# Performance work log

Hardware: AMD Instinct MI355X
Metric: run time of the kernel (lower is better)

## Reference

```python
import jax, jax.numpy as jnp
import numpy as np

N_NODES = 100000
N_EDGES = 6400000
N_FEAT = 128
HIDDEN = 16
N_CLASSES = 10
N_GRAPHS = 1024


def setup_inputs() -> dict:
    key = jax.random.key(0)
    ks = jax.random.split(key, 16)
    x = jax.random.normal(ks[0], (N_NODES, N_FEAT), dtype=jnp.float32)
    src = jax.random.randint(ks[1], (N_EDGES,), 0, N_NODES, dtype=jnp.int64)
    dst = jax.random.randint(ks[2], (N_EDGES,), 0, N_NODES, dtype=jnp.int64)
    edge_index = jnp.stack([src, dst], axis=0)
    batch = jnp.sort(jax.random.randint(ks[3], (N_NODES,), 0, N_GRAPHS, dtype=jnp.int64))
    s = 0.1
    emb = jax.random.normal(ks[4], (N_FEAT, HIDDEN), dtype=jnp.float32) * s
    W1l = jax.random.normal(ks[5], (HIDDEN, HIDDEN), dtype=jnp.float32) * s
    b1 = jnp.zeros((HIDDEN,), dtype=jnp.float32)
    W1r = jax.random.normal(ks[6], (HIDDEN, HIDDEN), dtype=jnp.float32) * s
    W2l = jax.random.normal(ks[7], (HIDDEN, HIDDEN), dtype=jnp.float32) * s
    b2 = jnp.zeros((HIDDEN,), dtype=jnp.float32)
    W2r = jax.random.normal(ks[8], (HIDDEN, HIDDEN), dtype=jnp.float32) * s
    W3l = jax.random.normal(ks[9], (N_CLASSES, HIDDEN), dtype=jnp.float32) * s
    b3 = jnp.zeros((N_CLASSES,), dtype=jnp.float32)
    W3r = jax.random.normal(ks[10], (N_CLASSES, HIDDEN), dtype=jnp.float32) * s
    return {"x": x, "edge_index": edge_index, "batch": batch, "emb": emb,
            "W1l": W1l, "b1": b1, "W1r": W1r,
            "W2l": W2l, "b2": b2, "W2r": W2r,
            "W3l": W3l, "b3": b3, "W3r": W3r}


def _sage_conv(h, src, dst, Wl, bl, Wr, n_nodes):
    # PyG SAGEConv (aggr='mean'): out = lin_l(mean_j x_j) + lin_r(x_i), then L2-normalize
    msgs = h[src]                                             # [E, F]
    agg = jax.ops.segment_sum(msgs, dst, num_segments=n_nodes)
    deg = jax.ops.segment_sum(jnp.ones((src.shape[0],), h.dtype), dst, num_segments=n_nodes)
    agg = agg / jnp.maximum(deg, 1.0)[:, None]
    out = agg @ Wl.T + bl + h @ Wr.T
    norm = jnp.linalg.norm(out, axis=-1, keepdims=True)
    return out / jnp.maximum(norm, 1e-12)


def reference(x, edge_index, batch, emb, W1l, b1, W1r, W2l, b2, W2r, W3l, b3, W3r):
    src, dst = edge_index[0], edge_index[1]
    n = x.shape[0]
    # embedding of argmax over one-hot-ish features
    h = emb[jnp.argmax(x, axis=1)]                            # [N, H]
    h = jax.nn.relu(_sage_conv(h, src, dst, W1l, b1, W1r, n))  # dropout is identity in eval
    h = jax.nn.relu(_sage_conv(h, src, dst, W2l, b2, W2r, n))
    h = _sage_conv(h, src, dst, W3l, b3, W3r, n)              # [N, C]
    # global mean pool over graphs
    pooled = jax.ops.segment_sum(h, batch, num_segments=N_GRAPHS)
    cnt = jax.ops.segment_sum(jnp.ones((n,), h.dtype), batch, num_segments=N_GRAPHS)
    pooled = pooled / jnp.maximum(cnt, 1.0)[:, None]
    return jax.nn.softmax(pooled, axis=1)
```

## Files before the change

kernel.cpp:

```cpp
#include <hip/hip_runtime.h>
#include <hip/hip_bf16.h>

#define N_FEAT 128
#define HID 16
#define NCLS 10
#define NGRAPH 1024
#define SHIFT 7
#define NBMAX 1024
#define CAP 9216
#define CH 8192
#define EPB (CH / 256)
#define EPB2 (CH / 512)
#define GC_NODES 64
#define GCAP2 5120

__device__ __forceinline__ float u2f(unsigned int u) {
    union { unsigned int u; float f; } c; c.u = u; return c.f;
}
__device__ __forceinline__ float bf2f(__hip_bfloat16 b) {
    return __bfloat162float(b);
}
__device__ __forceinline__ unsigned short f2us(float f) {
    union { __hip_bfloat16 b; unsigned short u; } c;
    c.b = __float2bfloat16(f);
    return c.u;
}
__device__ __forceinline__ float ldw(const void* __restrict__ p, int i, int isbf) {
    return isbf ? bf2f(((const __hip_bfloat16*)p)[i]) : ((const float*)p)[i];
}
__device__ __forceinline__ void unp8(uint4 v, float* f) {
    f[0] = u2f(v.x << 16); f[1] = u2f(v.x & 0xffff0000u);
    f[2] = u2f(v.y << 16); f[3] = u2f(v.y & 0xffff0000u);
    f[4] = u2f(v.z << 16); f[5] = u2f(v.z & 0xffff0000u);
    f[6] = u2f(v.w << 16); f[7] = u2f(v.w & 0xffff0000u);
}
__device__ __forceinline__ void acc8(uint4 v, float* a8) {
    a8[0] += u2f(v.x << 16); a8[1] += u2f(v.x & 0xffff0000u);
    a8[2] += u2f(v.y << 16); a8[3] += u2f(v.y & 0xffff0000u);
    a8[4] += u2f(v.z << 16); a8[5] += u2f(v.z & 0xffff0000u);
    a8[6] += u2f(v.w << 16); a8[7] += u2f(v.w & 0xffff0000u);
}

__global__ void k_detect(const int* __restrict__ ei,
                         const unsigned int* __restrict__ xw,
                         int* __restrict__ flags) {
    if (blockIdx.x == 0 && threadIdx.x == 0) {
        int nz = 0;
        for (int i = 1; i < 256; i += 2) nz |= ei[i];
        flags[0] = (nz == 0) ? 1 : 0;
        int cnt = 0;
        for (int i = 0; i < 64; i++) {
            unsigned int ef = xw[i] & 0x7F80u;
            if (ef >= 0x3C00u && ef <= 0x4080u) cnt++;
        }
        flags[1] = (cnt >= 32) ? 1 : 0;
    }
}

__global__ void k_argmax_embed(const void* __restrict__ x,
                               const void* __restrict__ emb,
                               const int* __restrict__ flags,
                               unsigned short* __restrict__ h, int n) {
    int wave = (int)((blockIdx.x * (unsigned)blockDim.x + threadIdx.x) >> 6);
    int lane = threadIdx.x & 63;
    if (wave >= n) return;
    int isbf = flags[1];
    float v0, v1;
    if (isbf) {
        const unsigned int* row =
            (const unsigned int*)((const __hip_bfloat16*)x + (size_t)wave * N_FEAT);
        unsigned int u = row[lane];
        v0 = u2f(u << 16);
        v1 = u2f(u & 0xffff0000u);
    } else {
        const float2* row = (const float2*)((const float*)x + (size_t)wave * N_FEAT);
        float2 u = row[lane];
        v0 = u.x; v1 = u.y;
    }
    float bv; int bi;
    if (v1 > v0) { bv = v1; bi = 2 * lane + 1; }
    else         { bv = v0; bi = 2 * lane; }
    #pragma unroll
    for (int off = 1; off < 64; off <<= 1) {
        float ov = __shfl_xor(bv, off);
        int   oi = __shfl_xor(bi, off);
        if (ov > bv || (ov == bv && oi < bi)) { bv = ov; bi = oi; }
    }
    if (lane < HID) {
        unsigned short us;
        if (isbf) us = ((const unsigned short*)emb)[bi * HID + lane];
        else      us = f2us(((const float*)emb)[bi * HID + lane]);
        h[(size_t)wave * HID + lane] = us;
    }
}

__global__ void k_binhist(const int* __restrict__ ei, const int* __restrict__ flags,
                          int* __restrict__ rbBuf, int e, int nbins) {
    __shared__ int lh[NBMAX];
    int t = threadIdx.x;
    for (int b = t; b < nbins; b += 256) lh[b] = 0;
    __syncthreads();
    int base = blockIdx.x * CH;
    int sh = flags[0];
    for (int j = 0; j < EPB; j++) {
        int i = base + j * 256 + t;
        if (i < e) {
            int d = ei[((size_t)(e + i)) << sh];
            atomicAdd(&lh[d >> SHIFT], 1);
        }
    }
    __syncthreads();
    int* row = rbBuf + (size_t)blockIdx.x * nbins;
    for (int b = t; b < nbins; b += 256) row[b] = lh[b];
}

__global__ void k_colscan(int* __restrict__ rbBuf, int* __restrict__ binCnt,
                          int nblk, int nbins) {
    __shared__ int ls[1024];
    int b = blockIdx.x, t = threadIdx.x;
    int v = (t < nblk) ? rbBuf[(size_t)t * nbins + b] : 0;
    ls[t] = v;
    __syncthreads();
    #pragma unroll
    for (int off = 1; off < 1024; off <<= 1) {
        int w = (t >= off) ? ls[t - off] : 0;
        __syncthreads();
        ls[t] += w;
        __syncthreads();
    }
    if (t < nblk) rbBuf[(size_t)t * nbins + b] = ls[t] - v;
    if (t == 1023) binCnt[b] = ls[t];
}

__global__ void k_scanbins(const int* __restrict__ binCnt,
                           int* __restrict__ binStart, int nbins, int e) {
    __shared__ int ls[1024];
    int t = threadIdx.x;
    int v = (t < nbins) ? binCnt[t] : 0;
    ls[t] = v;
    __syncthreads();
    #pragma unroll
    for (int off = 1; off < 1024; off <<= 1) {
        int w = (t >= off) ? ls[t - off] : 0;
        __syncthreads();
        ls[t] += w;
        __syncthreads();
    }
    if (t < nbins) binStart[t] = ls[t] - v;
    if (t == 0) binStart[nbins] = e;
}

__global__ __launch_bounds__(512) void k_binplace(
        const int* __restrict__ ei, const int* __restrict__ flags,
        const int* __restrict__ binStart, const int* __restrict__ rbBuf,
        int* __restrict__ col, int e, int nbins) {
    __shared__ int cnt[NBMAX];
    __shared__ int ldsOff[NBMAX];
    __shared__ int ldsBase[NBMAX];
    __shared__ int ps[512];
    __shared__ int stage[CH];
    __shared__ unsigned short binOf[CH];
    int t = threadIdx.x;
    for (int b = t; b < nbins; b += 512) cnt[b] = 0;
    __syncthreads();
    int base = blockIdx.x * CH;
    int sh = flags[0];
    int myV[EPB2]; short myB[EPB2];
    for (int j = 0; j < EPB2; j++) {
        int i = base + j * 512 + t;
        if (i < e) {
            int s = ei[((size_t)i) << sh];
            int d = ei[((size_t)(e + i)) << sh];
            myV[j] = (s << SHIFT) | (d & ((1 << SHIFT) - 1));
            int b2 = d >> SHIFT;
            myB[j] = (short)b2;
            atomicAdd(&cnt[b2], 1);
        } else myB[j] = -1;
    }
    __syncthreads();
    int c[2]; int lsum = 0;
    int bb = t * 2;
    #pragma unroll
    for (int k = 0; k < 2; k++) {
        int b2 = bb + k;
        c[k] = (b2 < nbins) ? cnt[b2] : 0;
        lsum += c[k];
    }
    ps[t] = lsum;
    __syncthreads();
    #pragma unroll
    for (int off = 1; off < 512; off <<= 1) {
        int w = (t >= off) ? ps[t - off] : 0;
        __syncthreads();
        ps[t] += w;
        __syncthreads();
    }
    int run = ps[t] - lsum;
    #pragma unroll
    for (int k = 0; k < 2; k++) {
        int b2 = bb + k;
        if (b2 < nbins) ldsOff[b2] = run;
        run += c[k];
    }
    __syncthreads();
    const int* rb = rbBuf + (size_t)blockIdx.x * nbins;
    for (int b2 = t; b2 < nbins; b2 += 512) {
        ldsBase[b2] = binStart[b2] + rb[b2] - ldsOff[b2];
        cnt[b2] = 0;
    }
    __syncthreads();
    for (int j = 0; j < EPB2; j++) {
        if (myB[j] >= 0) {
            int b2 = myB[j];
            int r = atomicAdd(&cnt[b2], 1);
            int p = ldsOff[b2] + r;
            stage[p] = myV[j];
            binOf[p] = (unsigned short)b2;
        }
    }
    __syncthreads();
    int total = e - base;
    if (total > CH) total = CH;
    for (int i = t; i < total; i += 512) {
        int b2 = binOf[i];
        col[ldsBase[b2] + i] = stage[i];
    }
}

__global__ __launch_bounds__(512) void k_place(
        int* __restrict__ col, const int* __restrict__ binStart,
        int* __restrict__ rowStart, int n, int e) {
    __shared__ int stage[CAP];
    __shared__ int cntN[1 << SHIFT];
    __shared__ int sc[1 << SHIFT];
    __shared__ int rs[1 << SHIFT];
    int b = blockIdx.x;
    int t = threadIdx.x;
    int nb = b << SHIFT;
    int s0 = binStart[b];
    int s1 = binStart[b + 1];
    int cnt = s1 - s0;
    if (t < (1 << SHIFT)) cntN[t] = 0;
    bool st = (cnt <= CAP);
    __syncthreads();
    for (int i = t; i < cnt; i += 512) {
        int v = col[s0 + i];
        if (st) stage[i] = v;
        atomicAdd(&cntN[v & ((1 << SHIFT) - 1)], 1);
    }
    __syncthreads();
    if (t < (1 << SHIFT)) sc[t] = cntN[t];
    __syncthreads();
    #pragma unroll
    for (int off = 1; off < (1 << SHIFT); off <<= 1) {
        int w = 0;
        if (t < (1 << SHIFT) && t >= off) w = sc[t - off];
        __syncthreads();
        if (t < (1 << SHIFT)) sc[t] += w;
        __syncthreads();
    }
    if (t < (1 << SHIFT)) {
        int start = s0 + sc[t] - cntN[t];
        rs[t] = start;
        int node = nb + t;
        if (node < n) rowStart[node] = start;
        cntN[t] = 0;
    }
    __syncthreads();
    for (int i = t; i < cnt; i += 512) {
        int v = st ? stage[i] : col[s0 + i];
        int dl = v & ((1 << SHIFT) - 1);
        int r = atomicAdd(&cntN[dl], 1);
        col[rs[dl] + r] = v >> SHIFT;
    }
}

__global__ __launch_bounds__(256) void k_gc(
        const int* __restrict__ col, const int* __restrict__ rowStart,
        const unsigned short* __restrict__ hin,
        const void* __restrict__ Wl, const void* __restrict__ bia,
        const void* __restrict__ Wr, const int* __restrict__ flags,
        unsigned short* __restrict__ hout, int n, int e) {
    __shared__ int ecol[GCAP2];
    __shared__ float wl[HID][HID], wr[HID][HID], bb[HID];
    int t = threadIdx.x;
    int b = blockIdx.x;
    int isbf = flags[1];
    if (t < HID * HID) {
        wl[t >> 4][t & 15] = ldw(Wl, t, isbf);
        wr[t >> 4][t & 15] = ldw(Wr, t, isbf);
    }
    if (t < HID) bb[t] = ldw(bia, t, isbf);
    int nb = b * GC_NODES;
    int s0 = rowStart[nb];
    int s1 = (nb + GC_NODES < n) ? rowStart[nb + GC_NODES] : e;
    int nl = t >> 2;
    int q  = t & 3;
    int node = nb + nl;
    bool act = (node < n);
    int lo = 0, hi = 0;
    if (act) {
        lo = rowStart[node];
        hi = (node + 1 < n) ? rowStart[node + 1] : e;
    }
    const uint4* h4 = (const uint4*)hin;
    uint4 sv0, sv1;
    if (act && q == 0) {
        sv0 = h4[(size_t)node * 2];
        sv1 = h4[(size_t)node * 2 + 1];
    }
    int cnt = s1 - s0;
    bool st = (cnt <= GCAP2);
    if (st)
        for (int i = t; i < cnt; i += 256)
            ecol[i] = __builtin_nontemporal_load(col + s0 + i);
    __syncthreads();
    if (!act) return;

    float a16[16];
    #pragma unroll
    for (int k = 0; k < 16; k++) a16[k] = 0.0f;
    if (st) {
        int i = lo - s0 + q;
        int end = hi - s0;
        for (; i + 12 < end; i += 16) {
            int e0 = ecol[i], e1 = ecol[i + 4], e2 = ecol[i + 8], e3 = ecol[i + 12];
            uint4 va0 = h4[(size_t)e0 * 2],     vb0 = h4[(size_t)e0 * 2 + 1];
            uint4 va1 = h4[(size_t)e1 * 2],     vb1 = h4[(size_t)e1 * 2 + 1];
            uint4 va2 = h4[(size_t)e2 * 2],     vb2 = h4[(size_t)e2 * 2 + 1];
            uint4 va3 = h4[(size_t)e3 * 2],     vb3 = h4[(size_t)e3 * 2 + 1];
            acc8(va0, a16); acc8(vb0, a16 + 8);
            acc8(va1, a16); acc8(vb1, a16 + 8);
            acc8(va2, a16); acc8(vb2, a16 + 8);
            acc8(va3, a16); acc8(vb3, a16 + 8);
        }
        for (; i < end; i += 4) {
            int s = ecol[i];
            uint4 va = h4[(size_t)s * 2], vb = h4[(size_t)s * 2 + 1];
            acc8(va, a16); acc8(vb, a16 + 8);
        }
    } else {
        int i = lo + q;
        for (; i + 12 < hi; i += 16) {
            int e0 = col[i], e1 = col[i + 4], e2 = col[i + 8], e3 = col[i + 12];
            uint4 va0 = h4[(size_t)e0 * 2],     vb0 = h4[(size_t)e0 * 2 + 1];
            uint4 va1 = h4[(size_t)e1 * 2],     vb1 = h4[(size_t)e1 * 2 + 1];
            uint4 va2 = h4[(size_t)e2 * 2],     vb2 = h4[(size_t)e2 * 2 + 1];
            uint4 va3 = h4[(size_t)e3 * 2],     vb3 = h4[(size_t)e3 * 2 + 1];
            acc8(va0, a16); acc8(vb0, a16 + 8);
            acc8(va1, a16); acc8(vb1, a16 + 8);
            acc8(va2, a16); acc8(vb2, a16 + 8);
            acc8(va3, a16); acc8(vb3, a16 + 8);
        }
        for (; i < hi; i += 4) {
            int s = col[i];
            uint4 va = h4[(size_t)s * 2], vb = h4[(size_t)s * 2 + 1];
            acc8(va, a16); acc8(vb, a16 + 8);
        }
    }
    #pragma unroll
    for (int k = 0; k < 16; k++) a16[k] += __shfl_xor(a16[k], 1);
    #pragma unroll
    for (int k = 0; k < 16; k++) a16[k] += __shfl_xor(a16[k], 2);
    if (q == 0) {
        float invd = 1.0f / fmaxf((float)(hi - lo), 1.0f);
        #pragma unroll
        for (int k = 0; k < 16; k++) a16[k] *= invd;
        float hb[HID];
        unp8(sv0, hb);
        unp8(sv1, hb + 8);
        float o[HID]; float sq = 0.0f;
        #pragma unroll
        for (int f = 0; f < HID; f++) {
            float acc = bb[f];
            #pragma unroll
            for (int k = 0; k < HID; k++)
                acc += a16[k] * wl[f][k] + hb[k] * wr[f][k];
            o[f] = acc;
            sq += acc * acc;
        }
        float inn = 1.0f / fmaxf(sqrtf(sq), 1e-12f);
        uint4 w0, w1;
        unsigned int* wp0 = (unsigned int*)&w0;
        unsigned int* wp1 = (unsigned int*)&w1;
        #pragma unroll
        for (int v = 0; v < 4; v++) {
            unsigned int l0 = f2us(fmaxf(o[2 * v] * inn, 0.0f));
            unsigned int h0 = f2us(fmaxf(o[2 * v + 1] * inn, 0.0f));
            wp0[v] = l0 | (h0 << 16);
            unsigned int l1 = f2us(fmaxf(o[8 + 2 * v] * inn, 0.0f));
            unsigned int h1 = f2us(fmaxf(o[8 + 2 * v + 1] * inn, 0.0f));
            wp1[v] = l1 | (h1 << 16);
        }
        ((uint4*)hout)[(size_t)node * 2]     = w0;
        ((uint4*)hout)[(size_t)node * 2 + 1] = w1;
    }
}

__global__ __launch_bounds__(256) void k_gc3(
        const int* __restrict__ col, const int* __restrict__ rowStart,
        const unsigned short* __restrict__ hin,
        const void* __restrict__ Wl, const void* __restrict__ bia,
        const void* __restrict__ Wr, const int* __restrict__ flags,
        float* __restrict__ h3, int n, int e) {
    __shared__ int ecol[GCAP2];
    __shared__ float wl[NCLS][HID], wr[NCLS][HID], bb[NCLS];
    int t = threadIdx.x;
    int b = blockIdx.x;
    int isbf = flags[1];
    if (t < NCLS * HID) {
        wl[t >> 4][t & 15] = ldw(Wl, t, isbf);
        wr[t >> 4][t & 15] = ldw(Wr, t, isbf);
    }
    if (t < NCLS) bb[t] = ldw(bia, t, isbf);
    int nb = b * GC_NODES;
    int s0 = rowStart[nb];
    int s1 = (nb + GC_NODES < n) ? rowStart[nb + GC_NODES] : e;
    int nl = t >> 2;
    int q  = t & 3;
    int node = nb + nl;
    bool act = (node < n);
    int lo = 0, hi = 0;
    if (act) {
        lo = rowStart[node];
        hi = (node + 1 < n) ? rowStart[node + 1] : e;
    }
    const uint4* h4 = (const uint4*)hin;
    uint4 sv0, sv1;
    if (act && q == 0) {
        sv0 = h4[(size_t)node * 2];
        sv1 = h4[(size_t)node * 2 + 1];
    }
    int cnt = s1 - s0;
    bool st = (cnt <= GCAP2);
    if (st)
        for (int i = t; i < cnt; i += 256)
            ecol[i] = __builtin_nontemporal_load(col + s0 + i);
    __syncthreads();
    if (!act) return;

    float a16[16];
    #pragma unroll
    for (int k = 0; k < 16; k++) a16[k] = 0.0f;
    if (st) {
        int i = lo - s0 + q;
        int end = hi - s0;
        for (; i + 12 < end; i += 16) {
            int e0 = ecol[i], e1 = ecol[i + 4], e2 = ecol[i + 8], e3 = ecol[i + 12];
            uint4 va0 = h4[(size_t)e0 * 2],     vb0 = h4[(size_t)e0 * 2 + 1];
            uint4 va1 = h4[(size_t)e1 * 2],     vb1 = h4[(size_t)e1 * 2 + 1];
            uint4 va2 = h4[(size_t)e2 * 2],     vb2 = h4[(size_t)e2 * 2 + 1];
            uint4 va3 = h4[(size_t)e3 * 2],     vb3 = h4[(size_t)e3 * 2 + 1];
            acc8(va0, a16); acc8(vb0, a16 + 8);
            acc8(va1, a16); acc8(vb1, a16 + 8);
            acc8(va2, a16); acc8(vb2, a16 + 8);
            acc8(va3, a16); acc8(vb3, a16 + 8);
        }
        for (; i < end; i += 4) {
            int s = ecol[i];
            uint4 va = h4[(size_t)s * 2], vb = h4[(size_t)s * 2 + 1];
            acc8(va, a16); acc8(vb, a16 + 8);
        }
    } else {
        int i = lo + q;
        for (; i + 12 < hi; i += 16) {
            int e0 = col[i], e1 = col[i + 4], e2 = col[i + 8], e3 = col[i + 12];
            uint4 va0 = h4[(size_t)e0 * 2],     vb0 = h4[(size_t)e0 * 2 + 1];
            uint4 va1 = h4[(size_t)e1 * 2],     vb1 = h4[(size_t)e1 * 2 + 1];
            uint4 va2 = h4[(size_t)e2 * 2],     vb2 = h4[(size_t)e2 * 2 + 1];
            uint4 va3 = h4[(size_t)e3 * 2],     vb3 = h4[(size_t)e3 * 2 + 1];
            acc8(va0, a16); acc8(vb0, a16 + 8);
            acc8(va1, a16); acc8(vb1, a16 + 8);
            acc8(va2, a16); acc8(vb2, a16 + 8);
            acc8(va3, a16); acc8(vb3, a16 + 8);
        }
        for (; i < hi; i += 4) {
            int s = col[i];
            uint4 va = h4[(size_t)s * 2], vb = h4[(size_t)s * 2 + 1];
            acc8(va, a16); acc8(vb, a16 + 8);
        }
    }
    #pragma unroll
    for (int k = 0; k < 16; k++) a16[k] += __shfl_xor(a16[k], 1);
    #pragma unroll
    for (int k = 0; k < 16; k++) a16[k] += __shfl_xor(a16[k], 2);
    if (q == 0) {
        float invd = 1.0f / fmaxf((float)(hi - lo), 1.0f);
        #pragma unroll
        for (int k = 0; k < 16; k++) a16[k] *= invd;
        float hb[HID];
        unp8(sv0, hb);
        unp8(sv1, hb + 8);
        float o[NCLS]; float sq = 0.0f;
        #pragma unroll
        for (int f = 0; f < NCLS; f++) {
            float acc = bb[f];
            #pragma unroll
            for (int k = 0; k < HID; k++)
                acc += a16[k] * wl[f][k] + hb[k] * wr[f][k];
            o[f] = acc;
            sq += acc * acc;
        }
        float inn = 1.0f / fmaxf(sqrtf(sq), 1e-12f);
        float* op = h3 + (size_t)node * NCLS;
        #pragma unroll
        for (int f = 0; f < NCLS; f++) op[f] = o[f] * inn;
    }
}

__device__ __forceinline__ int lbound(const int* __restrict__ a, int n, int key, int sh) {
    int lo = 0, hi = n;
    while (lo < hi) {
        int mid = (lo + hi) >> 1;
        if (a[((size_t)mid) << sh] < key) lo = mid + 1; else hi = mid;
    }
    return lo;
}

__global__ void k_pool_softmax(const float* __restrict__ h3,
                               const int* __restrict__ batch,
                               const int* __restrict__ flags,
                               void* __restrict__ out, int n) {
    int g = blockIdx.x;
    int lane = threadIdx.x;
    int sh = flags[0];
    int lo = lbound(batch, n, g, sh);
    int hi = lbound(batch, n, g + 1, sh);
    float acc[NCLS];
    #pragma unroll
    for (int c = 0; c < NCLS; c++) acc[c] = 0.0f;
    for (int i = lo + lane; i < hi; i += 64) {
        const float* r = h3 + (size_t)i * NCLS;
        #pragma unroll
        for (int c = 0; c < NCLS; c++) acc[c] += r[c];
    }
    #pragma unroll
    for (int c = 0; c < NCLS; c++) {
        #pragma unroll
        for (int off = 1; off < 64; off <<= 1)
            acc[c] += __shfl_xor(acc[c], off);
    }
    float invc = 1.0f / fmaxf((float)(hi - lo), 1.0f);
    float m = -1e30f;
    #pragma unroll
    for (int c = 0; c < NCLS; c++) { acc[c] *= invc; m = fmaxf(m, acc[c]); }
    float s = 0.0f;
    #pragma unroll
    for (int c = 0; c < NCLS; c++) { acc[c] = expf(acc[c] - m); s += acc[c]; }
    float invs = 1.0f / s;
    if (lane < NCLS) {
        float v = acc[lane] * invs;
        size_t idx = (size_t)g * NCLS + lane;
        if (flags[1]) ((__hip_bfloat16*)out)[idx] = __float2bfloat16(v);
        else          ((float*)out)[idx] = v;
    }
}

extern "C" void kernel_launch(void* const* d_in, const int* in_sizes, int n_in,
                              void* d_out, int out_size, void* d_ws, size_t ws_size,
                              hipStream_t stream) {
    const void* x   = d_in[0];
    const int*  ei  = (const int*)d_in[1];
    const int*  bat = (const int*)d_in[2];
    const void* emb = d_in[3];
    const void* W1l = d_in[4];  const void* b1 = d_in[5];  const void* W1r = d_in[6];
    const void* W2l = d_in[7];  const void* b2 = d_in[8];  const void* W2r = d_in[9];
    const void* W3l = d_in[10]; const void* b3 = d_in[11]; const void* W3r = d_in[12];

    int n = in_sizes[0] / N_FEAT;
    int e = in_sizes[1] / 2;
    int nbins = (n + (1 << SHIFT) - 1) >> SHIFT;
    int nblk  = (e + CH - 1) / CH;

    unsigned short* hcur  = (unsigned short*)d_ws;
    unsigned short* hnext = hcur + (size_t)n * HID;
    float* h3       = (float*)(hnext + (size_t)n * HID);
    int*   col      = (int*)(h3 + (size_t)n * NCLS);
    int*   rowStart = col + e;
    int*   binCnt   = rowStart + n;
    int*   binStart = binCnt + nbins;
    int*   rbBuf    = binStart + (nbins + 1);
    int*   flags    = rbBuf + (size_t)nblk * nbins;

    int ngrid4 = (n + 3) / 4;
    int ngc = (n + GC_NODES - 1) / GC_NODES;

    k_detect<<<1, 64, 0, stream>>>(ei, (const unsigned int*)x, flags);
    k_binhist<<<nblk, 256, 0, stream>>>(ei, flags, rbBuf, e, nbins);
    k_colscan<<<nbins, 1024, 0, stream>>>(rbBuf, binCnt, nblk, nbins);
    k_scanbins<<<1, 1024, 0, stream>>>(binCnt, binStart, nbins, e);
    k_binplace<<<nblk, 512, 0, stream>>>(ei, flags, binStart, rbBuf, col, e, nbins);
    k_place<<<nbins, 512, 0, stream>>>(col, binStart, rowStart, n, e);

    k_argmax_embed<<<ngrid4, 256, 0, stream>>>(x, emb, flags, hcur, n);

    k_gc <<<ngc, 256, 0, stream>>>(col, rowStart, hcur,  W1l, b1, W1r, flags, hnext, n, e);
    k_gc <<<ngc, 256, 0, stream>>>(col, rowStart, hnext, W2l, b2, W2r, flags, hcur,  n, e);
    k_gc3<<<ngc, 256, 0, stream>>>(col, rowStart, hcur,  W3l, b3, W3r, flags, h3,    n, e);

    k_pool_softmax<<<NGRAPH, 64, 0, stream>>>(h3, bat, flags, d_out, n);
}
```

Baseline: 423.4 us.

## Replace per-block bin histogram scan with global atomic cursors; two nodes per wave in argmax

The binning stage no longer writes a per-block histogram matrix and column-scans it. Each block now atomically adds its local counts into a global bin count, and during placement it reserves output ranges through per-bin atomic cursors. This removes the k_colscan launch and the rbBuf traffic. The catch is that edge order within a bin now depends on block scheduling, so results can differ slightly from run to run. Separately, argmax_embed handles two nodes per wave using vector loads of four elements per lane, which halves the shuffle reduction depth per node.

After: 428.8 us. About the same (+1.3%).

```diff
diff --git a/kernel.cpp b/kernel.cpp
--- a/kernel.cpp
+++ b/kernel.cpp
@@ -9,7 +9,6 @@
 #define NBMAX 1024
 #define CAP 9216
 #define CH 8192
-#define EPB (CH / 256)
 #define EPB2 (CH / 512)
 #define GC_NODES 64
 #define GCAP2 5120
@@ -43,8 +42,11 @@
 
 __global__ void k_detect(const int* __restrict__ ei,
                          const unsigned int* __restrict__ xw,
-                         int* __restrict__ flags) {
-    if (blockIdx.x == 0 && threadIdx.x == 0) {
+                         int* __restrict__ flags,
+                         int* __restrict__ binCnt, int nbins) {
+    int t = threadIdx.x;
+    for (int b = t; b < nbins; b += 1024) binCnt[b] = 0;
+    if (t == 0) {
         int nz = 0;
         for (int i = 1; i < 256; i += 2) nz |= ei[i];
         flags[0] = (nz == 0) ? 1 : 0;
@@ -63,62 +65,67 @@
                                unsigned short* __restrict__ h, int n) {
     int wave = (int)((blockIdx.x * (unsigned)blockDim.x + threadIdx.x) >> 6);
     int lane = threadIdx.x & 63;
-    if (wave >= n) return;
+    int half = lane >> 5;
+    int l = lane & 31;
+    int node = wave * 2 + half;
+    if (node >= n) return;
     int isbf = flags[1];
-    float v0, v1;
+    float v[4];
     if (isbf) {
-        const unsigned int* row =
-            (const unsigned int*)((const __hip_bfloat16*)x + (size_t)wave * N_FEAT);
-        unsigned int u = row[lane];
-        v0 = u2f(u << 16);
-        v1 = u2f(u & 0xffff0000u);
+        uint2 u = ((const uint2*)((const __hip_bfloat16*)x + (size_t)node * N_FEAT))[l];
+        v[0] = u2f(u.x << 16); v[1] = u2f(u.x & 0xffff0000u);
+        v[2] = u2f(u.y << 16); v[3] = u2f(u.y & 0xffff0000u);
     } else {
-        const float2* row = (const float2*)((const float*)x + (size_t)wave * N_FEAT);
-        float2 u = row[lane];
-        v0 = u.x; v1 = u.y;
-    }
-    float bv; int bi;
-    if (v1 > v0) { bv = v1; bi = 2 * lane + 1; }
-    else         { bv = v0; bi = 2 * lane; }
-    #pragma unroll
-    for (int off = 1; off < 64; off <<= 1) {
+        float4 u = ((const float4*)((const float*)x + (size_t)node * N_FEAT))[l];
+        v[0] = u.x; v[1] = u.y; v[2] = u.z; v[3] = u.w;
+    }
+    float bv = v[0]; int bi = 4 * l;
+    #pragma unroll
+    for (int k = 1; k < 4; k++)
+        if (v[k] > bv) { bv = v[k]; bi = 4 * l + k; }
+    #pragma unroll
+    for (int off = 1; off < 32; off <<= 1) {
         float ov = __shfl_xor(bv, off);
         int   oi = __shfl_xor(bi, off);
         if (ov > bv || (ov == bv && oi < bi)) { bv = ov; bi = oi; }
     }
-    if (lane < HID) {
+    if (l < HID) {
         unsigned short us;
-        if (isbf) us = ((const unsigned short*)emb)[bi * HID + lane];
-        else      us = f2us(((const float*)emb)[bi * HID + lane]);
-        h[(size_t)wave * HID + lane] = us;
-    }
-}
-
-__global__ void k_binhist(const int* __restrict__ ei, const int* __restrict__ flags,
-                          int* __restrict__ rbBuf, int e, int nbins) {
+        if (isbf) us = ((const unsigned short*)emb)[bi * HID + l];
+        else      us = f2us(((const float*)emb)[bi * HID + l]);
+        h[(size_t)node * HID + l] = us;
+    }
+}
+
+__global__ __launch_bounds__(512) void k_binhist(
+        const int* __restrict__ ei, const int* __restrict__ flags,
+        int* __restrict__ binCnt, int e, int nbins) {
     __shared__ int lh[NBMAX];
     int t = threadIdx.x;
-    for (int b = t; b < nbins; b += 256) lh[b] = 0;
+    for (int b = t; b < nbins; b += 512) lh[b] = 0;
     __syncthreads();
     int base = blockIdx.x * CH;
     int sh = flags[0];
-    for (int j = 0; j < EPB; j++) {
-        int i = base + j * 256 + t;
+    for (int j = 0; j < EPB2; j++) {
+        int i = base + j * 512 + t;
         if (i < e) {
             int d = ei[((size_t)(e + i)) << sh];
             atomicAdd(&lh[d >> SHIFT], 1);
         }
     }
     __syncthreads();
-    int* row = rbBuf + (size_t)blockIdx.x * nbins;
-    for (int b = t; b < nbins; b += 256) row[b] = lh[b];
-}
-
-__global__ void k_colscan(int* __restrict__ rbBuf, int* __restrict__ binCnt,
-                          int nblk, int nbins) {
+    for (int b = t; b < nbins; b += 512) {
+        int c = lh[b];
+        if (c) atomicAdd(&binCnt[b], c);
+    }
+}
+
+__global__ void k_scanbins(const int* __restrict__ binCnt,
+                           int* __restrict__ binStart,
+                           int* __restrict__ cursor, int nbins, int e) {
     __shared__ int ls[1024];
-    int b = blockIdx.x, t = threadIdx.x;
-    int v = (t < nblk) ? rbBuf[(size_t)t * nbins + b] : 0;
+    int t = threadIdx.x;
+    int v = (t < nbins) ? binCnt[t] : 0;
     ls[t] = v;
     __syncthreads();
     #pragma unroll
@@ -128,31 +135,17 @@
         ls[t] += w;
         __syncthreads();
     }
-    if (t < nblk) rbBuf[(size_t)t * nbins + b] = ls[t] - v;
-    if (t == 1023) binCnt[b] = ls[t];
-}
-
-__global__ void k_scanbins(const int* __restrict__ binCnt,
-                           int* __restrict__ binStart, int nbins, int e) {
-    __shared__ int ls[1024];
-    int t = threadIdx.x;
-    int v = (t < nbins) ? binCnt[t] : 0;
-    ls[t] = v;
-    __syncthreads();
-    #pragma unroll
-    for (int off = 1; off < 1024; off <<= 1) {
-        int w = (t >= off) ? ls[t - off] : 0;
-        __syncthreads();
-        ls[t] += w;
-        __syncthreads();
-    }
-    if (t < nbins) binStart[t] = ls[t] - v;
+    if (t < nbins) {
+        int s = ls[t] - v;
+        binStart[t] = s;
+        cursor[t] = s;
+    }
     if (t == 0) binStart[nbins] = e;
 }
 
 __global__ __launch_bounds__(512) void k_binplace(
         const int* __restrict__ ei, const int* __restrict__ flags,
-        const int* __restrict__ binStart, const int* __restrict__ rbBuf,
+        int* __restrict__ cursor,
         int* __restrict__ col, int e, int nbins) {
     __shared__ int cnt[NBMAX];
     __shared__ int ldsOff[NBMAX];
@@ -199,14 +192,15 @@
     #pragma unroll
     for (int k = 0; k < 2; k++) {
         int b2 = bb + k;
-        if (b2 < nbins) ldsOff[b2] = run;
+        if (b2 < nbins) {
+            ldsOff[b2] = run;
+            if (c[k] > 0) {
+                int g = atomicAdd(&cursor[b2], c[k]);
+                ldsBase[b2] = g - run;
+            }
+            cnt[b2] = 0;
+        }
         run += c[k];
-    }
-    __syncthreads();
-    const int* rb = rbBuf + (size_t)blockIdx.x * nbins;
-    for (int b2 = t; b2 < nbins; b2 += 512) {
-        ldsBase[b2] = binStart[b2] + rb[b2] - ldsOff[b2];
-        cnt[b2] = 0;
     }
     __syncthreads();
     for (int j = 0; j < EPB2; j++) {
@@ -579,20 +573,19 @@
     int*   rowStart = col + e;
     int*   binCnt   = rowStart + n;
     int*   binStart = binCnt + nbins;
-    int*   rbBuf    = binStart + (nbins + 1);
-    int*   flags    = rbBuf + (size_t)nblk * nbins;
-
-    int ngrid4 = (n + 3) / 4;
+    int*   cursor   = binStart + (nbins + 1);
+    int*   flags    = cursor + nbins;
+
+    int ngridA = (n + 7) / 8;
     int ngc = (n + GC_NODES - 1) / GC_NODES;
 
-    k_detect<<<1, 64, 0, stream>>>(ei, (const unsigned int*)x, flags);
-    k_binhist<<<nblk, 256, 0, stream>>>(ei, flags, rbBuf, e, nbins);
-    k_colscan<<<nbins, 1024, 0, stream>>>(rbBuf, binCnt, nblk, nbins);
-    k_scanbins<<<1, 1024, 0, stream>>>(binCnt, binStart, nbins, e);
-    k_binplace<<<nblk, 512, 0, stream>>>(ei, flags, binStart, rbBuf, col, e, nbins);
+    k_detect<<<1, 1024, 0, stream>>>(ei, (const unsigned int*)x, flags, binCnt, nbins);
+    k_binhist<<<nblk, 512, 0, stream>>>(ei, flags, binCnt, e, nbins);
+    k_scanbins<<<1, 1024, 0, stream>>>(binCnt, binStart, cursor, nbins, e);
+    k_binplace<<<nblk, 512, 0, stream>>>(ei, flags, cursor, col, e, nbins);
     k_place<<<nbins, 512, 0, stream>>>(col, binStart, rowStart, n, e);
 
-    k_argmax_embed<<<ngrid4, 256, 0, stream>>>(x, emb, flags, hcur, n);
+    k_argmax_embed<<<ngridA, 256, 0, stream>>>(x, emb, flags, hcur, n);
 
     k_gc <<<ngc, 256, 0, stream>>>(col, rowStart, hcur,  W1l, b1, W1r, flags, hnext, n, e);
     k_gc <<<ngc, 256, 0, stream>>>(col, rowStart, hnext, W2l, b2, W2r, flags, hcur,  n, e);
```
